# Kernel optimization log

Hardware: AMD Instinct MI355X
Metric: run time of the kernel (lower is better)

## Reference

```python
import jax, jax.numpy as jnp
import numpy as np

CUTOFF = 5.0
MAX_K = 32
N_ATOMS = 100000
N_EDGES = 3200000


def setup_inputs() -> dict:
    key = jax.random.key(0)
    k1, k2 = jax.random.split(key)
    vectors = jax.random.normal(k1, (N_EDGES, 3), dtype=jnp.float32)
    first_atom = jax.random.randint(k2, (N_EDGES,), 0, N_ATOMS)
    return {"vectors": vectors, "first_atom": first_atom, "n_atoms": N_ATOMS}


def reference(vectors, first_atom, n_atoms):
    # per-edge distance, normalized by cutoff  [E]
    r = jnp.linalg.norm(vectors, axis=1) / CUTOFF
    # power basis r^k for k in [0, MAX_K)  [E, MAX_K]
    powers = r[:, None] ** jnp.arange(MAX_K, dtype=r.dtype)
    # fused edge->atom scatter-add over all k at once  [n_atoms, MAX_K]
    features = jax.ops.segment_sum(powers, first_atom, num_segments=n_atoms)
    # center by GLOBAL scalar mean (matches features_tensor - features_tensor.mean())
    centered = features - features.mean()
    _, _, Vt = jnp.linalg.svd(centered, full_matrices=False)
    # project UNcentered features onto top-3 right singular vectors  [n_atoms, 3]
    features_pca = features @ Vt[:3].T
    return features_pca
```

## Files before the change

### kernel.cpp

```cpp
#include <hip/hip_runtime.h>
#include <math.h>

#define MAX_K 32
#define CUTOFF 5.0f

#define SIGN0 -1.0f
#define SIGN1 -1.0f
#define SIGN2 -1.0f


__global__ __launch_bounds__(256) void r_hist_kernel(const float* __restrict__ vec,
                                                     const int* __restrict__ atom,
                                                     float* __restrict__ r_all,
                                                     int* __restrict__ count, int E) {
  int e = blockIdx.x * blockDim.x + threadIdx.x;
  if (e >= E) return;
  float x = __builtin_nontemporal_load(&vec[3 * e + 0]);
  float y = __builtin_nontemporal_load(&vec[3 * e + 1]);
  float z = __builtin_nontemporal_load(&vec[3 * e + 2]);
  float r = sqrtf(x * x + y * y + z * z) * (1.0f / CUTOFF);
  int rank = atomicAdd(&count[atom[e]], 1);
  unsigned u = (__float_as_uint(r) & 0xFFFFFF00u) | (unsigned)(rank & 0xFF);
  r_all[e] = __uint_as_float(u);
}

__global__ __launch_bounds__(1024) void bsum_kernel(const int* __restrict__ count,
                                                    int* __restrict__ bsum, int n) {
  __shared__ int red[1024];
  int t = threadIdx.x;
  int i = blockIdx.x * 1024 + t;
  red[t] = (i < n) ? count[i] : 0;
  __syncthreads();
  for (int d = 512; d > 0; d >>= 1) {
    if (t < d) red[t] += red[t + d];
    __syncthreads();
  }
  if (t == 0) bsum[blockIdx.x] = red[0];
}

__global__ __launch_bounds__(1024) void bscan_kernel(const int* __restrict__ bsum,
                                                     int* __restrict__ bbase, int nb) {
  __shared__ int v[1024];
  int t = threadIdx.x;
  v[t] = (t < nb) ? bsum[t] : 0;
  __syncthreads();
  if (t == 0) {
    int run = 0;
    for (int i = 0; i < nb; ++i) { int c = v[i]; v[i] = run; run += c; }
  }
  __syncthreads();
  if (t < nb) bbase[t] = v[t];
}

__global__ __launch_bounds__(1024) void apply_kernel(const int* __restrict__ count,
                                                     const int* __restrict__ bbase,
                                                     int* __restrict__ offset, int n) {
  __shared__ int part[1024];
  int t = threadIdx.x;
  int i = blockIdx.x * 1024 + t;
  int x = (i < n) ? count[i] : 0;
  part[t] = x;
  __syncthreads();
  for (int d = 1; d < 1024; d <<= 1) {
    int add = (t >= d) ? part[t - d] : 0;
    __syncthreads();
    part[t] += add;
    __syncthreads();
  }
  int excl = part[t] - x + bbase[blockIdx.x];
  if (i < n) offset[i] = excl;
}

__global__ __launch_bounds__(256) void scatter_rank_kernel(
    const float* __restrict__ r_all, const int* __restrict__ atom,
    const int* __restrict__ offset, float* __restrict__ sr, int E) {
  int e = blockIdx.x * blockDim.x + threadIdx.x;
  if (e >= E) return;
  unsigned u = __float_as_uint(__builtin_nontemporal_load(&r_all[e]));
  int a = __builtin_nontemporal_load(&atom[e]);
  int dst = offset[a] + (int)(u & 0xFFu);
  sr[dst] = __uint_as_float(u);
}

__global__ __launch_bounds__(256) void build_kernel(const float* __restrict__ sr,
                                                    const int* __restrict__ offset,
                                                    const int* __restrict__ count,
                                                    float* __restrict__ F, int n) {
  int a = blockIdx.x * blockDim.x + threadIdx.x;
  if (a >= n) return;
  float acc[MAX_K];
#pragma unroll
  for (int k = 0; k < MAX_K; ++k) acc[k] = 0.f;
  int o = offset[a], c = count[a];
  for (int i = 0; i < c; ++i) {
    float r = sr[o + i];
    float p = 1.f;
#pragma unroll
    for (int k = 0; k < MAX_K; ++k) { acc[k] += p; p *= r; }
  }
  float4* out = (float4*)(F + (size_t)a * MAX_K);
#pragma unroll
  for (int k4 = 0; k4 < 8; ++k4)
    out[k4] = make_float4(acc[4 * k4], acc[4 * k4 + 1], acc[4 * k4 + 2], acc[4 * k4 + 3]);
}

__global__ __launch_bounds__(256) void edge_kernel(const float* __restrict__ vec,
                                                   const int* __restrict__ atom,
                                                   float* __restrict__ F, int E) {
  int e = blockIdx.x * blockDim.x + threadIdx.x;
  if (e >= E) return;
  float x = vec[3 * e + 0], y = vec[3 * e + 1], z = vec[3 * e + 2];
  float r = sqrtf(x * x + y * y + z * z) * (1.0f / CUTOFF);
  float* out = F + (size_t)atom[e] * MAX_K;
  float p = 1.0f;
#pragma unroll
  for (int k = 0; k < MAX_K; ++k) {
    atomicAdd(out + k, p);
    p *= r;
  }
}

__global__ __launch_bounds__(256) void gram_kernel(const float* __restrict__ F, int n,
                                                   double* __restrict__ G,
                                                   double* __restrict__ S) {
  __shared__ float rows[8][MAX_K];
  int tid = threadIdx.x;
  int pi[3], pj[3];
  int npair = 0;
  for (int p = tid; p < 528; p += 256) {
    int i = 0, pp = p;
    while (pp >= MAX_K - i) { pp -= (MAX_K - i); i++; }
    pi[npair] = i;
    pj[npair] = i + pp;
    npair++;
  }
  double acc[3] = {0.0, 0.0, 0.0};
  double colsum = 0.0;
  int nchunk = (n + 7) / 8;
  int row = tid >> 5, col = tid & 31;
  for (int ch = blockIdx.x; ch < nchunk; ch += gridDim.x) {
    int a = ch * 8 + row;
    rows[row][col] = (a < n) ? F[(size_t)a * MAX_K + col] : 0.0f;
    __syncthreads();
#pragma unroll
    for (int r = 0; r < 8; ++r) {
      for (int t = 0; t < npair; ++t)
        acc[t] += (double)rows[r][pi[t]] * (double)rows[r][pj[t]];
      if (tid < MAX_K) colsum += (double)rows[r][tid];
    }
    __syncthreads();
  }
  for (int t = 0; t < npair; ++t) atomicAdd(&G[pi[t] * MAX_K + pj[t]], acc[t]);
  if (tid < MAX_K) atomicAdd(&S[tid], colsum);
}

__global__ __launch_bounds__(256) void eig_kernel(const double* __restrict__ Gin,
                                                  const double* __restrict__ S,
                                                  float* __restrict__ V3, int n_atoms) {
  __shared__ float A[32][33];
  __shared__ float V[32][33];
  __shared__ float rcs[16], rss[16];
  __shared__ double wred[4];
  __shared__ int sel[3];
  __shared__ double ssign[3];
  int t = threadIdx.x;
  int ki = t >> 4;
  int kj = t & 15;

  double stot = 0.0;
  for (int k = 0; k < 32; ++k) stot += S[k];
  double mu = stot / ((double)n_atoms * 32.0);

  for (int idx = t; idx < 1024; idx += 256) {
    int i = idx >> 5, j = idx & 31;
    double g = (i <= j) ? Gin[i * 32 + j] : Gin[j * 32 + i];
    A[i][j] = (float)(g - mu * (S[i] + S[j]) + mu * mu * (double)n_atoms);
    V[i][j] = (i == j) ? 1.0f : 0.0f;
  }
  __syncthreads();

  double part = 0.0;
  for (int idx = t; idx < 1024; idx += 256) {
    int i = idx >> 5, j = idx & 31;
    part += (double)A[i][j] * (double)A[i][j];
  }
  for (int o = 32; o; o >>= 1) part += __shfl_xor(part, o, 64);
  if ((t & 63) == 0) wred[t >> 6] = part;
  __syncthreads();
  double fro2 = wred[0] + wred[1] + wred[2] + wred[3];
  float fro_f = (float)sqrt(fro2);
  float skip_thr = 1e-7f * fro_f;
  double off_tol2 = fro2 * 1e-12;
  __syncthreads();

  int q0 = 0;
  int ai_ = ki, bi_ = (ki == 0) ? 0 : (31 - ki);
  int aj_ = kj, bj_ = (kj == 0) ? 0 : (31 - kj);
  int ma = (t < 16) ? t : 0;
  int mb = (t >= 1 && t < 16) ? (31 - t) : 0;

  for (int sweep = 0; sweep < 8; ++sweep) {
    double off = 0.0;
    for (int idx = t; idx < 1024; idx += 256) {
      int i = idx >> 5, j = idx & 31;
      if (i != j) off += (double)A[i][j] * (double)A[i][j];
    }
    for (int o = 32; o; o >>= 1) off += __shfl_xor(off, o, 64);
    if ((t & 63) == 0) wred[t >> 6] = off;
    __syncthreads();
    double offT = wred[0] + wred[1] + wred[2] + wred[3];
    __syncthreads();
    if (offT <= off_tol2) break;

    for (int r = 0; r < 31; ++r) {
      if (t < 16) {
        float cf = 1.0f, sf = 0.0f;
        int p, q;
        if (t == 0) { p = 31; q = q0; }
        else { p = (ma < mb) ? ma : mb; q = (ma < mb) ? mb : ma; }
        float apq = A[p][q];
        if (fabsf(apq) > skip_thr) {
          float app = A[p][p], aqq = A[q][q];
          float tau = (aqq - app) / (2.0f * apq);
          float tt = 1.0f / (fabsf(tau) + sqrtf(1.0f + tau * tau));
          if (tau < 0.0f) tt = -tt;
          cf = 1.0f / sqrtf(1.0f + tt * tt);
          sf = tt * cf;
        }
        rcs[t] = cf; rss[t] = sf;
      }
      __syncthreads();

      int pi_, qi_, pj_, qj_;
      if (ki == 0) { pi_ = 31; qi_ = q0; }
      else { pi_ = (ai_ < bi_) ? ai_ : bi_; qi_ = (ai_ < bi_) ? bi_ : ai_; }
      if (kj == 0) { pj_ = 31; qj_ = q0; }
      else { pj_ = (aj_ < bj_) ? aj_ : bj_; qj_ = (aj_ < bj_) ? bj_ : aj_; }
      float ci = rcs[ki], si = rss[ki];
      float cj = rcs[kj], sj = rss[kj];
      float m00 = A[pi_][pj_], m01 = A[pi_][qj_];
      float m10 = A[qi_][pj_], m11 = A[qi_][qj_];
      float r00 = ci * m00 - si * m10, r01 = ci * m01 - si * m11;
      float r10 = si * m00 + ci * m10, r11 = si * m01 + ci * m11;
      A[pi_][pj_] = cj * r00 - sj * r01;
      A[pi_][qj_] = sj * r00 + cj * r01;
      A[qi_][pj_] = cj * r10 - sj * r11;
      A[qi_][qj_] = sj * r10 + cj * r11;
      float v00 = V[pi_][pj_], v01 = V[pi_][qj_];
      float v10 = V[qi_][pj_], v11 = V[qi_][qj_];
      V[pi_][pj_] = cj * v00 - sj * v01;
      V[pi_][qj_] = sj * v00 + cj * v01;
      V[qi_][pj_] = cj * v10 - sj * v11;
      V[qi_][qj_] = sj * v10 + cj * v11;
      __syncthreads();

      ai_ = (ai_ == 30) ? 0 : ai_ + 1;
      bi_ = (bi_ == 30) ? 0 : bi_ + 1;
      aj_ = (aj_ == 30) ? 0 : aj_ + 1;
      bj_ = (bj_ == 30) ? 0 : bj_ + 1;
      ma = (ma == 30) ? 0 : ma + 1;
      mb = (mb == 30) ? 0 : mb + 1;
      q0 = (q0 == 30) ? 0 : q0 + 1;
    }
  }
  __syncthreads();

  if (t == 0) {
    bool used[32];
    for (int i = 0; i < 32; ++i) used[i] = false;
    for (int j = 0; j < 3; ++j) {
      int best = 0; float bv = -1e30f;
      for (int i = 0; i < 32; ++i)
        if (!used[i] && A[i][i] > bv) { bv = A[i][i]; best = i; }
      used[best] = true;
      sel[j] = best;
      int m = 0; float mv = fabsf(V[0][best]);
      for (int i = 1; i < 32; ++i) {
        float av = fabsf(V[i][best]);
        if (av > mv) { mv = av; m = i; }
      }
      ssign[j] = (V[m][best] < 0.0f) ? -1.0 : 1.0;
    }
  }
  __syncthreads();
  const float adj[3] = {SIGN0, SIGN1, SIGN2};
  if (t < 32) {
    for (int j = 0; j < 3; ++j)
      V3[j * 32 + t] = (float)ssign[j] * V[t][sel[j]] * adj[j];
  }
}

__global__ __launch_bounds__(256) void proj_kernel(const float* __restrict__ F,
                                                   const float* __restrict__ V3,
                                                   float* __restrict__ out, int n) {
  __shared__ float v[96];
  if (threadIdx.x < 96) v[threadIdx.x] = V3[threadIdx.x];
  __syncthreads();
  int a = blockIdx.x * blockDim.x + threadIdx.x;
  if (a >= n) return;
  const float4* rowp = (const float4*)(F + (size_t)a * 32);
  float s0 = 0.f, s1 = 0.f, s2 = 0.f;
#pragma unroll
  for (int k4 = 0; k4 < 8; ++k4) {
    float4 f = rowp[k4];
    int k = k4 * 4;
    s0 += f.x * v[k] + f.y * v[k + 1] + f.z * v[k + 2] + f.w * v[k + 3];
    s1 += f.x * v[32 + k] + f.y * v[32 + k + 1] + f.z * v[32 + k + 2] + f.w * v[32 + k + 3];
    s2 += f.x * v[64 + k] + f.y * v[64 + k + 1] + f.z * v[64 + k + 2] + f.w * v[64 + k + 3];
  }
  out[3 * a + 0] = s0;
  out[3 * a + 1] = s1;
  out[3 * a + 2] = s2;
}

extern "C" void kernel_launch(void* const* d_in, const int* in_sizes, int n_in,
                              void* d_out, int out_size, void* d_ws, size_t ws_size,
                              hipStream_t stream) {
  const float* vec = (const float*)d_in[0];
  const int* atom = (const int*)d_in[1];
  int E = in_sizes[1];
  int n_atoms = out_size / 3;
  int nb = (n_atoms + 1023) >> 10;

  char* ws = (char*)d_ws;
  auto nalign = [](size_t x) { return (x + 255) & ~(size_t)255; };

  size_t F_bytes = (size_t)n_atoms * MAX_K * sizeof(float);
  size_t sr_bytes = (size_t)E * sizeof(float);
  size_t i_bytes = (size_t)n_atoms * sizeof(int);

  size_t F_off = 0;
  size_t sr_off = nalign(F_off + F_bytes);
  size_t offs_off = nalign(sr_off + sr_bytes);
  size_t cur_off = nalign(offs_off + i_bytes);
  size_t cnt_off = nalign(cur_off + i_bytes);
  size_t G_off = nalign(cnt_off + i_bytes);
  size_t S_off = nalign(G_off + 1024 * sizeof(double));
  size_t bs_off = nalign(S_off + 32 * sizeof(double));
  size_t bb_off = nalign(bs_off + 1024 * sizeof(int));
  size_t V3_off = nalign(bb_off + 1024 * sizeof(int));
  size_t total = nalign(V3_off + 96 * sizeof(float));

  float* F = (float*)(ws + F_off);
  double* G = (double*)(ws + G_off);
  double* S = (double*)(ws + S_off);
  float* V3 = (float*)(ws + V3_off);

  float* r_all = F;

  if (ws_size >= total && sr_bytes <= F_bytes) {
    float* sr = (float*)(ws + sr_off);
    int* offset = (int*)(ws + offs_off);
    int* count = (int*)(ws + cnt_off);
    int* bsum = (int*)(ws + bs_off);
    int* bbase = (int*)(ws + bb_off);
    hipMemsetAsync(ws + cnt_off, 0, S_off + 32 * sizeof(double) - cnt_off, stream);
    r_hist_kernel<<<(E + 255) / 256, 256, 0, stream>>>(vec, atom, r_all, count, E);
    bsum_kernel<<<nb, 1024, 0, stream>>>(count, bsum, n_atoms);
    bscan_kernel<<<1, 1024, 0, stream>>>(bsum, bbase, nb);
    apply_kernel<<<nb, 1024, 0, stream>>>(count, bbase, offset, n_atoms);
    scatter_rank_kernel<<<(E + 255) / 256, 256, 0, stream>>>(r_all, atom, offset, sr, E);
    build_kernel<<<(n_atoms + 255) / 256, 256, 0, stream>>>(sr, offset, count, F, n_atoms);
    gram_kernel<<<1024, 256, 0, stream>>>(F, n_atoms, G, S);
    eig_kernel<<<1, 256, 0, stream>>>(G, S, V3, n_atoms);
    proj_kernel<<<(n_atoms + 255) / 256, 256, 0, stream>>>(F, V3, (float*)d_out, n_atoms);
  } else {
    hipMemsetAsync(ws, 0, F_bytes, stream);
    hipMemsetAsync(ws + cnt_off, 0, S_off + 32 * sizeof(double) - cnt_off, stream);
    edge_kernel<<<(E + 255) / 256, 256, 0, stream>>>(vec, atom, F, E);
    gram_kernel<<<1024, 256, 0, stream>>>(F, n_atoms, G, S);
    eig_kernel<<<1, 256, 0, stream>>>(G, S, V3, n_atoms);
    proj_kernel<<<(n_atoms + 255) / 256, 256, 0, stream>>>(F, V3, (float*)d_out, n_atoms);
  }
}
```

Baseline: 386.1 us.

## Fuse feature build with Gram matrix accumulation via shared-memory tile

Merges the per-atom feature build and the separate Gram/column-sum kernel into one kernel. Each block stages its 256 feature rows in shared memory and computes the 528 upper-triangle pair products and the column sums in double, then adds them to global G and S with atomics. This avoids re-reading F from memory and saves one launch, at the cost of per-block double atomics and a serial 256-row loop. The atom index load in the histogram kernel is also made nontemporal.

New measurement: 440.8 us. 1.14x slower.

```diff
diff --git a/kernel.cpp b/kernel.cpp
--- a/kernel.cpp
+++ b/kernel.cpp
@@ -19,7 +19,8 @@
   float y = __builtin_nontemporal_load(&vec[3 * e + 1]);
   float z = __builtin_nontemporal_load(&vec[3 * e + 2]);
   float r = sqrtf(x * x + y * y + z * z) * (1.0f / CUTOFF);
-  int rank = atomicAdd(&count[atom[e]], 1);
+  int a = __builtin_nontemporal_load(&atom[e]);
+  int rank = atomicAdd(&count[a], 1);
   unsigned u = (__float_as_uint(r) & 0xFFFFFF00u) | (unsigned)(rank & 0xFF);
   r_all[e] = __uint_as_float(u);
 }
@@ -82,26 +83,53 @@
   sr[dst] = __uint_as_float(u);
 }
 
-__global__ __launch_bounds__(256) void build_kernel(const float* __restrict__ sr,
-                                                    const int* __restrict__ offset,
-                                                    const int* __restrict__ count,
-                                                    float* __restrict__ F, int n) {
-  int a = blockIdx.x * blockDim.x + threadIdx.x;
-  if (a >= n) return;
+__global__ __launch_bounds__(256) void buildgram_kernel(const float* __restrict__ sr,
+                                                        const int* __restrict__ offset,
+                                                        const int* __restrict__ count,
+                                                        float* __restrict__ F,
+                                                        double* __restrict__ G,
+                                                        double* __restrict__ S, int n) {
+  __shared__ float rows[256][MAX_K + 1];
+  int tid = threadIdx.x;
+  int a = blockIdx.x * 256 + tid;
   float acc[MAX_K];
 #pragma unroll
   for (int k = 0; k < MAX_K; ++k) acc[k] = 0.f;
-  int o = offset[a], c = count[a];
-  for (int i = 0; i < c; ++i) {
-    float r = sr[o + i];
-    float p = 1.f;
-#pragma unroll
-    for (int k = 0; k < MAX_K; ++k) { acc[k] += p; p *= r; }
-  }
-  float4* out = (float4*)(F + (size_t)a * MAX_K);
-#pragma unroll
-  for (int k4 = 0; k4 < 8; ++k4)
-    out[k4] = make_float4(acc[4 * k4], acc[4 * k4 + 1], acc[4 * k4 + 2], acc[4 * k4 + 3]);
+  if (a < n) {
+    int o = offset[a], c = count[a];
+    for (int i = 0; i < c; ++i) {
+      float r = sr[o + i];
+      float p = 1.f;
+#pragma unroll
+      for (int k = 0; k < MAX_K; ++k) { acc[k] += p; p *= r; }
+    }
+    float4* out = (float4*)(F + (size_t)a * MAX_K);
+#pragma unroll
+    for (int k4 = 0; k4 < 8; ++k4)
+      out[k4] = make_float4(acc[4 * k4], acc[4 * k4 + 1], acc[4 * k4 + 2], acc[4 * k4 + 3]);
+  }
+#pragma unroll
+  for (int k = 0; k < MAX_K; ++k) rows[tid][k] = acc[k];
+  __syncthreads();
+
+  int pi[3], pj[3];
+  int npair = 0;
+  for (int p = tid; p < 528; p += 256) {
+    int i = 0, pp = p;
+    while (pp >= MAX_K - i) { pp -= (MAX_K - i); i++; }
+    pi[npair] = i;
+    pj[npair] = i + pp;
+    npair++;
+  }
+  double accp[3] = {0.0, 0.0, 0.0};
+  double colsum = 0.0;
+  for (int r = 0; r < 256; ++r) {
+    for (int t = 0; t < npair; ++t)
+      accp[t] += (double)rows[r][pi[t]] * (double)rows[r][pj[t]];
+    if (tid < MAX_K) colsum += (double)rows[r][tid];
+  }
+  for (int t = 0; t < npair; ++t) atomicAdd(&G[pi[t] * MAX_K + pj[t]], accp[t]);
+  if (tid < MAX_K) atomicAdd(&S[tid], colsum);
 }
 
 __global__ __launch_bounds__(256) void edge_kernel(const float* __restrict__ vec,
@@ -360,8 +388,7 @@
     bscan_kernel<<<1, 1024, 0, stream>>>(bsum, bbase, nb);
     apply_kernel<<<nb, 1024, 0, stream>>>(count, bbase, offset, n_atoms);
     scatter_rank_kernel<<<(E + 255) / 256, 256, 0, stream>>>(r_all, atom, offset, sr, E);
-    build_kernel<<<(n_atoms + 255) / 256, 256, 0, stream>>>(sr, offset, count, F, n_atoms);
-    gram_kernel<<<1024, 256, 0, stream>>>(F, n_atoms, G, S);
+    buildgram_kernel<<<(n_atoms + 255) / 256, 256, 0, stream>>>(sr, offset, count, F, G, S, n_atoms);
     eig_kernel<<<1, 256, 0, stream>>>(G, S, V3, n_atoms);
     proj_kernel<<<(n_atoms + 255) / 256, 256, 0, stream>>>(F, V3, (float*)d_out, n_atoms);
   } else {
```
